# Optimization experiments

Hardware: AMD Instinct MI355X
Metric: run time of the kernel (lower is better)

Reference implementation:

```python
import jax, jax.numpy as jnp
import numpy as np

B, S, D, H = 4, 1024, 1024, 16
HD = D // H          # head space dim = 64
FF = 4 * D           # ffn hidden = 4096
EPS = 1e-6

# ---- Lorentz manifold helpers (curvature k=1: -t^2 + |s|^2 = -1) ----

def to_manifold(space):
    t = jnp.sqrt(jnp.sum(space * space, -1, keepdims=True) + 1.0)
    return jnp.concatenate([t, space], -1)

def l_inner(x, y):
    return -x[..., 0] * y[..., 0] + jnp.sum(x[..., 1:] * y[..., 1:], -1)

def project(z):
    # renormalize onto hyperboloid: z / sqrt(|<z,z>_L|)   (Lorentz midpoint / LResNet)
    d = jnp.sqrt(jnp.clip(-l_inner(z, z), EPS))
    return z / d[..., None]

def hyp_layernorm(x, g, b):
    s = x[..., 1:]
    mu = jnp.mean(s, -1, keepdims=True)
    var = jnp.var(s, -1, keepdims=True)
    s = (s - mu) * jax.lax.rsqrt(var + 1e-5) * g + b
    return to_manifold(s)

def apply_rope(xs, cos, sin):
    # xs [B,S,H,HD]; cos/sin [S,HD//2]; freqs broadcast as [1,S,1,HD//2]
    x2 = xs.reshape(*xs.shape[:-1], HD // 2, 2)
    c = cos[None, :, None, :]
    s = sin[None, :, None, :]
    xr = x2[..., 0] * c - x2[..., 1] * s
    xi = x2[..., 0] * s + x2[..., 1] * c
    return jnp.stack([xr, xi], -1).reshape(xs.shape)


def setup_inputs() -> dict:
    key = jax.random.key(0)
    ks = jax.random.split(key, 8)
    def w(k, shape, fan_in):
        return jax.random.normal(k, shape, jnp.float32) / np.sqrt(fan_in).astype(np.float32)
    x = to_manifold(0.5 * jax.random.normal(ks[0], (B, S, D), jnp.float32))
    pos = jnp.arange(S, dtype=jnp.float32)[:, None]
    inv = 1.0 / (10000.0 ** (jnp.arange(0, HD, 2, dtype=jnp.float32) / HD))
    ang = pos * inv[None, :]
    return {
        'x': x,
        'rope_cos': jnp.cos(ang), 'rope_sin': jnp.sin(ang),
        'norm1_g': jnp.ones((D,), jnp.float32), 'norm1_b': jnp.zeros((D,), jnp.float32),
        'Wq': w(ks[1], (H, D + 1, HD), D + 1), 'bq': jnp.zeros((H, HD), jnp.float32),
        'Wk': w(ks[2], (H, D + 1, HD), D + 1), 'bk': jnp.zeros((H, HD), jnp.float32),
        'Wv': w(ks[3], (H, D + 1, HD), D + 1), 'bv': jnp.zeros((H, HD), jnp.float32),
        'attn_scale': jnp.asarray(np.sqrt(HD), jnp.float32),
        'attn_bias': jnp.zeros((), jnp.float32),
        'Wo': w(ks[4], (H * (HD + 1), D), H * (HD + 1)), 'bo': jnp.zeros((D,), jnp.float32),
        'w_res1': jnp.asarray(1.0, jnp.float32),
        'norm2_g': jnp.ones((D,), jnp.float32), 'norm2_b': jnp.zeros((D,), jnp.float32),
        'W1': w(ks[5], (D + 1, FF), D + 1), 'b1': jnp.zeros((FF,), jnp.float32),
        'W2': w(ks[6], (FF + 1, D), FF + 1), 'b2': jnp.zeros((D,), jnp.float32),
        'w_res2': jnp.asarray(1.0, jnp.float32),
    }


def reference(x, rope_cos, rope_sin, norm1_g, norm1_b, Wq, bq, Wk, bk, Wv, bv,
              attn_scale, attn_bias, Wo, bo, w_res1, norm2_g, norm2_b,
              W1, b1, W2, b2, w_res2):
    # ---- pre-norm ----
    xn = hyp_layernorm(x, norm1_g, norm1_b)
    # ---- per-head Lorentz linear (space part), inline RoPE on q/k ----
    qs = jnp.einsum('bsd,hde->bshe', xn, Wq) + bq          # [B,S,H,HD]
    ksp = jnp.einsum('bsd,hde->bshe', xn, Wk) + bk
    vsp = jnp.einsum('bsd,hde->bshe', xn, Wv) + bv
    qs = apply_rope(qs, rope_cos, rope_sin)
    ksp = apply_rope(ksp, rope_cos, rope_sin)
    # hyperbolic normalization of q/k: unit space norm, time recomputed
    qs = qs * jax.lax.rsqrt(jnp.sum(qs * qs, -1, keepdims=True) + EPS)
    ksp = ksp * jax.lax.rsqrt(jnp.sum(ksp * ksp, -1, keepdims=True) + EPS)
    q = to_manifold(qs)                                    # [B,S,H,HD+1]
    k = to_manifold(ksp)
    v = to_manifold(vsp)
    # ---- curvature-aware scores: 2 + 2 <q,k>_L (neg sq Lorentz distance) ----
    sgn = jnp.concatenate([-jnp.ones((1,), q.dtype), jnp.ones((HD,), q.dtype)])
    cin = jnp.einsum('bshe,bthe->bhst', q * sgn, k)        # Minkowski inner [B,H,S,S]
    att = (2.0 + 2.0 * cin) / attn_scale + attn_bias
    P = jax.nn.softmax(att, axis=-1)
    # ---- Lorentz midpoint aggregation of values ----
    m = jnp.einsum('bhst,bthe->bshe', P, v)
    m = project(m)                                         # back onto hyperboloid
    # ---- heads concat + output Lorentz linear ----
    cat = m.reshape(B, S, H * (HD + 1))
    attn_out = to_manifold(cat @ Wo + bo)
    # ---- LResNet residual 1 ----
    x = project(x + w_res1 * attn_out)
    # ---- Lorentz FFN ----
    h = hyp_layernorm(x, norm2_g, norm2_b)
    h = to_manifold(jax.nn.gelu(h @ W1 + b1))
    mlp = to_manifold(h @ W2 + b2)
    # ---- LResNet residual 2 ----
    x = project(x + w_res2 * mlp)
    return x
```

## Files before the change

kernel.cpp:

```cpp
#include <hip/hip_runtime.h>
#include <hip/hip_bf16.h>

typedef __hip_bfloat16 bf16;
typedef __attribute__((ext_vector_type(8))) short short8;
typedef __attribute__((ext_vector_type(4))) float f32x4;

#define B_  4
#define S_  1024
#define H_  16
#define R_  4096
#define LD_ 1088

#define MBL 1048576L
#define OFF_WQKVT (0L)
#define OFF_WOT   (6684672L)
#define OFF_X2    (0L)
#define OFF_W1T   (9L*MBL)
#define OFF_W2T   (18L*MBL)
#define OFF_BIAS  (26L*MBL)
#define OFF_XNB   (27L*MBL + MBL/2)
#define OFF_MCAT  OFF_XNB
#define OFF_HBUF  OFF_XNB
#define OFF_QPS   (36L*MBL)
#define OFF_ARAW  OFF_QPS
#define OFF_KPS   (44L*MBL)
#define OFF_VT    (52L*MBL)
#define OFF_QT    (62L*MBL)
#define OFF_KT    (62L*MBL + 262144L)
#define OFF_HHBIG (44L*MBL)
#define OFF_MLPB  (76L*MBL)
#define OFF_HHC   (36L*MBL)
#define OFF_MLPF  (44L*MBL)
#define BQKV 0
#define BOF  16384
#define B1F  32768
#define B2F  65536
#define W2R0 81920
#define RCF  98304
#define RSNF 262144
#define SCLF 409600
#define TACC 425984
#define FLAG 458752

__device__ __forceinline__ bf16  f2bf(float v) { return __float2bfloat16(v); }
__device__ __forceinline__ float bf2f(bf16 v)  { return __bfloat162float(v); }
__device__ __forceinline__ unsigned short bf2s(float v) {
  return __builtin_bit_cast(unsigned short, __float2bfloat16(v));
}
__device__ __forceinline__ float ldu(const void* p, long i, int isbf) {
  return isbf ? bf2f(((const bf16*)p)[i]) : ((const float*)p)[i];
}
__device__ __forceinline__ void stu(void* p, long i, float v, int isbf) {
  if (isbf) ((bf16*)p)[i] = f2bf(v);
  else      ((float*)p)[i] = v;
}
__device__ __forceinline__ float gelu_f(float v) {
  const float u = 0.7978845608028654f * (v + 0.044715f * v * v * v);
  const float e = __expf(fminf(2.f * u, 80.f));
  return 0.5f * v * (1.f + (e - 1.f) / (e + 1.f));
}
__device__ __forceinline__ float bfu_lo(unsigned u) {
  return __builtin_bit_cast(float, u << 16);
}
__device__ __forceinline__ float bfu_hi(unsigned u) {
  return __builtin_bit_cast(float, u & 0xFFFF0000u);
}

__device__ __forceinline__ void gload16(const bf16* g, short* l) {
  __builtin_amdgcn_global_load_lds(
      (const __attribute__((address_space(1))) unsigned int*)g,
      (__attribute__((address_space(3))) unsigned int*)l, 16, 0, 0);
}

__global__ void detect_kernel(const unsigned* __restrict__ g, int* __restrict__ flag) {
  if (threadIdx.x == 0) flag[0] = (g[0] == 0x3F803F80u) ? 1 : 0;
}

__global__ __launch_bounds__(256) void zero16_kernel(uint4* __restrict__ p, int n16) {
  int i = blockIdx.x * 256 + threadIdx.x;
  if (i < n16) p[i] = uint4{0, 0, 0, 0};
}

__device__ __forceinline__ float bred_f(float v, float* sh) {
#pragma unroll
  for (int o = 32; o; o >>= 1) v += __shfl_xor(v, o);
  __syncthreads();
  if ((threadIdx.x & 63) == 0) sh[threadIdx.x >> 6] = v;
  __syncthreads();
  return sh[0] + sh[1] + sh[2] + sh[3];
}
__device__ __forceinline__ double bred_d(double v, double* sh) {
#pragma unroll
  for (int o = 32; o; o >>= 1) v += __shfl_xor(v, o);
  __syncthreads();
  if ((threadIdx.x & 63) == 0) sh[threadIdx.x >> 6] = v;
  __syncthreads();
  return sh[0] + sh[1] + sh[2] + sh[3];
}

__global__ __launch_bounds__(256) void mega_prep(
    const void* x, const void* rc, const void* rsn, const void* n1g, const void* n1b,
    const void* Wq, const void* bq, const void* Wk, const void* bk,
    const void* Wv, const void* bv, const void* scl, const void* ab,
    const void* Wo, const void* bo, const void* wr1,
    const void* W1, const void* b1, const void* W2, const void* b2, const void* wr2,
    char* bias_base, bf16* __restrict__ wqkvT, bf16* __restrict__ woT,
    bf16* __restrict__ w1T, bf16* __restrict__ w2T, bf16* __restrict__ xnb,
    const int* __restrict__ flag) {
  const int isbf = flag[0];
  __shared__ float tl[64][65];
  const int tid = threadIdx.x;
  int bid = blockIdx.x;
  if (bid < 297) {
    int i = bid * 256 + tid;
    float* bqkvf = (float*)(bias_base + BQKV);
    if (i < 1024)        { bqkvf[i] = ldu(bq, i, isbf); return; }
    if (i < 2048)        { bqkvf[i] = ldu(bk, i - 1024, isbf); return; }
    if (i < 3072)        { bqkvf[i] = ldu(bv, i - 2048, isbf); return; }
    if (i < 4096)        { ((float*)(bias_base + BOF))[i - 3072] = ldu(bo, i - 3072, isbf); return; }
    if (i < 8192)        { ((float*)(bias_base + B1F))[i - 4096] = ldu(b1, i - 4096, isbf); return; }
    if (i < 9216)        { ((float*)(bias_base + B2F))[i - 8192] = ldu(b2, i - 8192, isbf); return; }
    if (i < 10240)       { ((float*)(bias_base + W2R0))[i - 9216] = ldu(W2, i - 9216, isbf); return; }
    if (i < 10240+32768) { ((float*)(bias_base + RCF))[i - 10240] = ldu(rc, i - 10240, isbf); return; }
    if (i < 10240+65536) { ((float*)(bias_base + RSNF))[i - 43008] = ldu(rsn, i - 43008, isbf); return; }
    if (i == 75776)      { ((float*)(bias_base + SCLF))[0] = ldu(scl, 0, isbf); return; }
    if (i == 75777)      { ((float*)(bias_base + SCLF))[1] = ldu(ab, 0, isbf); return; }
    if (i == 75778)      { ((float*)(bias_base + SCLF))[2] = ldu(wr1, 0, isbf); return; }
    if (i == 75779)      { ((float*)(bias_base + SCLF))[3] = ldu(wr2, 0, isbf); return; }
    return;
  }
  bid -= 297;
  const int tx = tid & 63, tg = tid >> 6;
  if (bid < 816) {
    int k0 = (bid % 17) * 64, z = bid / 17;
    int mode = z >> 4, h = z & 15;
    const void* src = (mode == 0) ? Wq : (mode == 1) ? Wk : Wv;
    const long soff = (long)h * 1025 * 64;
    int base_n = mode * 1024 + h * 64;
    for (int i = tg; i < 64; i += 4) {
      int k = k0 + i;
      tl[i][tx] = (k < 1025) ? ldu(src, soff + (long)k * 64 + tx, isbf) : 0.f;
    }
    __syncthreads();
    for (int i = tg; i < 64; i += 4) {
      int k = k0 + tx;
      if (k < LD_) wqkvT[(long)(base_n + i) * LD_ + k] = f2bf(tl[tx][i]);
    }
    return;
  }
  bid -= 816;
  if (bid < 272) {
    int k0 = (bid % 17) * 64, n0 = (bid / 17) * 64;
    for (int i = tg; i < 64; i += 4) {
      int kp = k0 + i;
      float v = 0.f;
      if (kp < 1056) {
        int h = kp / 66, e = kp - h * 66;
        if (e < 65) v = ldu(Wo, (long)(h * 65 + e) * 1024 + n0 + tx, isbf);
      }
      tl[i][tx] = v;
    }
    __syncthreads();
    for (int i = tg; i < 64; i += 4) {
      int kp = k0 + tx;
      if (kp < LD_) woT[(long)(n0 + i) * LD_ + kp] = f2bf(tl[tx][i]);
    }
    return;
  }
  bid -= 272;
  if (bid < 1088) {
    int k0 = (bid % 17) * 64, n0 = (bid / 17) * 64;
    for (int i = tg; i < 64; i += 4) {
      int k = k0 + i;
      tl[i][tx] = (k < 1025) ? ldu(W1, (long)k * 4096 + n0 + tx, isbf) : 0.f;
    }
    __syncthreads();
    for (int i = tg; i < 64; i += 4) {
      int k = k0 + tx;
      if (k < LD_) w1T[(long)(n0 + i) * LD_ + k] = f2bf(tl[tx][i]);
    }
    return;
  }
  bid -= 1088;
  if (bid < 1024) {
    int k0 = (bid % 64) * 64, n0 = (bid / 64) * 64;
    for (int i = tg; i < 64; i += 4) {
      int k = k0 + i;
      tl[i][tx] = ldu(W2, 1024 + (long)k * 1024 + n0 + tx, isbf);
    }
    __syncthreads();
    for (int i = tg; i < 64; i += 4) {
      int k = k0 + tx;
      w2T[(long)(n0 + i) * 4096 + k] = f2bf(tl[tx][i]);
    }
    return;
  }
  bid -= 1024;
  {
    float* red = &tl[0][0];
    const long base = (long)bid * 1025;
    const long obase = (long)bid * LD_;
    float v[4];
#pragma unroll
    for (int i = 0; i < 4; i++) v[i] = ldu(x, base + 1 + tid * 4 + i, isbf);
    float s = 0.f, s2 = 0.f;
#pragma unroll
    for (int i = 0; i < 4; i++) { s += v[i]; s2 += v[i] * v[i]; }
    s  = bred_f(s,  red);
    s2 = bred_f(s2, red);
    const float mu  = s * (1.f / 1024.f);
    const float var = s2 * (1.f / 1024.f) - mu * mu;
    const float rs  = rsqrtf(var + 1e-5f);
    float n[4], ns = 0.f;
#pragma unroll
    for (int i = 0; i < 4; i++) {
      const int e = tid * 4 + i;
      n[i] = (v[i] - mu) * rs * ldu(n1g, e, isbf) + ldu(n1b, e, isbf);
      ns += n[i] * n[i];
    }
    ns = bred_f(ns, red);
    if (tid == 0) xnb[obase] = f2bf(sqrtf(ns + 1.f));
#pragma unroll
    for (int i = 0; i < 4; i++) xnb[obase + 1 + tid * 4 + i] = f2bf(n[i]);
    if (tid < 63) xnb[obase + 1025 + tid] = f2bf(0.f);
  }
}

__device__ __forceinline__ void gemm256_main(const bf16* __restrict__ A, int lda,
                                             const bf16* __restrict__ Bw, int ldb, int K,
                                             short (*__restrict__ As)[8192],
                                             short (*__restrict__ Bs)[8192],
                                             f32x4 (*acc)[4]) {
  const int tid = threadIdx.x, lane = tid & 63, wv = tid >> 6;
  const int quad = lane >> 4, q15 = lane & 15;
  const int wave_m = wv >> 2, wave_n = wv & 3;
  const int m0 = blockIdx.y * 256, n0 = blockIdx.x * 256;
  const int NT = K >> 5;
  const int u0 = tid, u1 = tid + 512;
  const int r0 = u0 >> 2, c0 = ((u0 & 3) ^ ((u0 >> 3) & 3)) * 8;
  const int r1 = u1 >> 2, c1 = ((u1 & 3) ^ ((u1 >> 3) & 3)) * 8;
  const bf16* pa0 = A + (long)(m0 + r0) * lda + c0;
  const bf16* pa1 = A + (long)(m0 + r1) * lda + c1;
  const bf16* pb0 = Bw + (long)(n0 + r0) * ldb + c0;
  const bf16* pb1 = Bw + (long)(n0 + r1) * ldb + c1;
  const int d0 = u0 * 8, d1 = u1 * 8;
  const int kswz = (quad ^ ((q15 >> 1) & 3)) * 8;
  const int arow = wave_m * 128 + q15;
  const int brow = wave_n * 64 + q15;
  gload16(pa0, As[0] + d0); gload16(pa1, As[0] + d1);
  gload16(pb0, Bs[0] + d0); gload16(pb1, Bs[0] + d1);
  pa0 += 32; pa1 += 32; pb0 += 32; pb1 += 32;
  gload16(pa0, As[1] + d0); gload16(pa1, As[1] + d1);
  gload16(pb0, Bs[1] + d0); gload16(pb1, Bs[1] + d1);
  pa0 += 32; pa1 += 32; pb0 += 32; pb1 += 32;
  asm volatile("s_waitcnt vmcnt(4)" ::: "memory");
  __builtin_amdgcn_s_barrier();
#pragma unroll 1
  for (int t = 0; t < NT; ++t) {
    const int buf = t & 3, sb = (t + 2) & 3;
    const short* ab = As[buf];
    const short* bb = Bs[buf];
    short8 af[4], bfr[4];
#pragma unroll
    for (int i = 0; i < 4; i++) {
      af[i]  = *(const short8*)(ab + (arow + i * 16) * 32 + kswz);
      bfr[i] = *(const short8*)(bb + (brow + i * 16) * 32 + kswz);
    }
    if (t + 2 < NT) {
      gload16(pa0, As[sb] + d0); gload16(pa1, As[sb] + d1);
      pa0 += 32; pa1 += 32;
    }
    __builtin_amdgcn_s_barrier();
    __builtin_amdgcn_s_setprio(1);
#pragma unroll
    for (int mi = 0; mi < 4; mi++)
#pragma unroll
      for (int ni = 0; ni < 4; ni++)
        acc[mi][ni] = __builtin_amdgcn_mfma_f32_16x16x32_bf16(af[mi], bfr[ni], acc[mi][ni], 0, 0, 0);
    __builtin_amdgcn_s_setprio(0);
    __builtin_amdgcn_s_barrier();
#pragma unroll
    for (int i = 0; i < 4; i++)
      af[i] = *(const short8*)(ab + (arow + 64 + i * 16) * 32 + kswz);
    if (t + 2 < NT) {
      gload16(pb0, Bs[sb] + d0); gload16(pb1, Bs[sb] + d1);
      pb0 += 32; pb1 += 32;
      asm volatile("s_waitcnt vmcnt(4)" ::: "memory");
    } else {
      asm volatile("s_waitcnt vmcnt(0)" ::: "memory");
    }
    __builtin_amdgcn_s_barrier();
    __builtin_amdgcn_s_setprio(1);
#pragma unroll
    for (int mi = 0; mi < 4; mi++)
#pragma unroll
      for (int ni = 0; ni < 4; ni++)
        acc[4 + mi][ni] = __builtin_amdgcn_mfma_f32_16x16x32_bf16(af[mi], bfr[ni], acc[4 + mi][ni], 0, 0, 0);
    __builtin_amdgcn_s_setprio(0);
    __builtin_amdgcn_s_barrier();
  }
}

template <int EPI>
__global__ __launch_bounds__(512) void gemm256(const bf16* __restrict__ A, int lda,
                                               const bf16* __restrict__ Bw, int ldb, int K,
                                               const float* __restrict__ bias,
                                               void* __restrict__ Cv, int ldc, int accf) {
  __shared__ __align__(16) short As[4][8192];
  __shared__ __align__(16) short Bs[4][8192];
  f32x4 acc[8][4] = {};
  gemm256_main(A, lda, Bw, ldb, K, As, Bs, acc);
  const int tid = threadIdx.x, lane = tid & 63, wv = tid >> 6;
  const int quad = lane >> 4, q15 = lane & 15;
  const int wave_m = wv >> 2, wave_n = wv & 3;
  const int m0 = blockIdx.y * 256, n0 = blockIdx.x * 256;
#pragma unroll
  for (int j = 0; j < 8; j++) {
#pragma unroll
    for (int r = 0; r < 4; r++) {
      const int m = m0 + wave_m * 128 + (j >> 2) * 64 + (j & 3) * 16 + quad * 4 + r;
#pragma unroll
      for (int ni = 0; ni < 4; ni++) {
        const int n = n0 + wave_n * 64 + ni * 16 + q15;
        float v = acc[j][ni][r] + (bias ? bias[n] : 0.f);
        const long idx = (long)m * ldc + n;
        if (EPI == 0) {
          float* Cf = (float*)Cv;
          if (accf) v += Cf[idx];
          Cf[idx] = v;
        } else if (EPI == 1) {
          ((bf16*)Cv)[idx] = f2bf(v);
        } else {
          ((bf16*)Cv)[idx] = f2bf(gelu_f(v));
        }
      }
    }
  }
}

__global__ __launch_bounds__(512) void gemm_qkv256(const bf16* __restrict__ A,
                                                   const bf16* __restrict__ Wt,
                                                   const char* __restrict__ bias_base,
                                                   bf16* __restrict__ qPs, float* __restrict__ qtc,
                                                   bf16* __restrict__ kPs, float* __restrict__ ktc,
                                                   bf16* __restrict__ vT) {
  __shared__ __align__(16) short As[4][8192];
  __shared__ __align__(16) short Bs[4][8192];
  f32x4 acc[8][4] = {};
  gemm256_main(A, LD_, Wt, LD_, LD_, As, Bs, acc);
  const int tid = threadIdx.x, lane = tid & 63, wv = tid >> 6;
  const int quad = lane >> 4, q15 = lane & 15;
  const int wave_m = wv >> 2, wave_n = wv & 3;
  const int m0 = blockIdx.y * 256, n0 = blockIdx.x * 256;
  const float* bqkvf = (const float*)(bias_base + BQKV);
  const float* rcf   = (const float*)(bias_base + RCF);
  const float* rsnf  = (const float*)(bias_base + RSNF);
  const int hg = (n0 >> 6) + wave_n;
  const int mode = hg >> 4, h = hg & 15;
  const int nb = hg * 64;
#pragma unroll
  for (int j = 0; j < 8; j++) {
#pragma unroll
    for (int r = 0; r < 4; r++) {
      const int m = m0 + wave_m * 128 + (j >> 2) * 64 + (j & 3) * 16 + quad * 4 + r;
      const int bb = m >> 10, s = m & 1023;
      const int bh = bb * H_ + h;
      float v[4];
#pragma unroll
      for (int ns = 0; ns < 4; ns++) v[ns] = acc[j][ns][r] + bqkvf[nb + ns * 16 + q15];
      if (mode < 2) {
#pragma unroll
        for (int ns = 0; ns < 4; ns++) {
          const int eg = ns * 16 + q15;
          const int jj = eg >> 1;
          const float c = rcf[s * 32 + jj], sn = rsnf[s * 32 + jj];
          const float p = __shfl_xor(v[ns], 1);
          v[ns] = ((eg & 1) == 0) ? (v[ns] * c - p * sn) : (p * sn + v[ns] * c);
        }
      }
      float ss = v[0] * v[0] + v[1] * v[1] + v[2] * v[2] + v[3] * v[3];
#pragma unroll
      for (int o = 8; o; o >>= 1) ss += __shfl_xor(ss, o);
      if (mode == 0) {
        const float sc = rsqrtf(ss + 1e-6f);
        const long rb2 = (long)(bh * 1024 + s) * 64;
#pragma unroll
        for (int ns = 0; ns < 4; ns++) qPs[rb2 + ns * 16 + q15] = f2bf(v[ns] * sc);
        if (q15 == 0) qtc[bh * 1024 + s] = sqrtf(ss / (ss + 1e-6f) + 1.f);
      } else if (mode == 1) {
        const float sc = rsqrtf(ss + 1e-6f);
        const long rb2 = (long)(bh * 1024 + s) * 64;
#pragma unroll
        for (int ns = 0; ns < 4; ns++) kPs[rb2 + ns * 16 + q15] = f2bf(v[ns] * sc);
        if (q15 == 0) ktc[bh * 1024 + s] = sqrtf(ss / (ss + 1e-6f) + 1.f);
      } else {
        const long vb = (long)bh * 81920;
#pragma unroll
        for (int ns = 0; ns < 4; ns++) vT[vb + (long)(1 + ns * 16 + q15) * 1024 + s] = f2bf(v[ns]);
        if (q15 == 0) vT[vb + s] = f2bf(sqrtf(ss + 1.f));
      }
    }
  }
}

template <int EPI, bool SS>
__global__ __launch_bounds__(256) void mfma_gemm(const bf16* __restrict__ A, int lda,
                                                 const bf16* __restrict__ Bw, int ldb, int K,
                                                 const float* __restrict__ bias,
                                                 void* __restrict__ Cv, int ldc, int accf,
                                                 float* __restrict__ tacc) {
  __shared__ __align__(16) short As[2][128 * 32];
  __shared__ __align__(16) short Bs[2][64 * 32];
  const int tid = threadIdx.x, lane = tid & 63, wv = tid >> 6;
  const int quad = lane >> 4, q15 = lane & 15;
  const int wave_m = wv & 1, wave_n = wv >> 1;
  const int n0 = blockIdx.x * 64, m0 = blockIdx.y * 128;
  const int sa0 = wv * 128 + lane, sa1 = sa0 + 64;
  const int ra0 = sa0 >> 2, ca0 = (sa0 & 3) ^ (ra0 & 3);
  const int ra1 = sa1 >> 2, ca1 = (sa1 & 3) ^ (ra1 & 3);
  const int rb = tid >> 2, cb = (tid & 3) ^ (rb & 3);
  const int kswz = (quad ^ (q15 & 3)) * 8;
  const bf16* pa0 = A + (long)(m0 + ra0) * lda + ca0 * 8;
  const bf16* pa1 = A + (long)(m0 + ra1) * lda + ca1 * 8;
  const bf16* pb  = Bw + (long)(n0 + rb) * ldb + cb * 8;
  f32x4 acc[4][2] = {};
  for (int k0 = 0; k0 < K; k0 += 64) {
#pragma unroll
    for (int p = 0; p < 2; p++) {
      gload16(pa0 + p * 32, As[p] + sa0 * 8);
      gload16(pa1 + p * 32, As[p] + sa1 * 8);
      gload16(pb + p * 32, Bs[p] + tid * 8);
    }
    pa0 += 64; pa1 += 64; pb += 64;
    __syncthreads();
#pragma unroll
    for (int p = 0; p < 2; p++) {
      short8 af[4], bfr[2];
#pragma unroll
      for (int i = 0; i < 4; i++)
        af[i] = *(const short8*)(As[p] + (wave_m * 64 + i * 16 + q15) * 32 + kswz);
#pragma unroll
      for (int i = 0; i < 2; i++)
        bfr[i] = *(const short8*)(Bs[p] + (wave_n * 32 + i * 16 + q15) * 32 + kswz);
#pragma unroll
      for (int mi = 0; mi < 4; mi++)
#pragma unroll
        for (int ni = 0; ni < 2; ni++)
          acc[mi][ni] = __builtin_amdgcn_mfma_f32_16x16x32_bf16(af[mi], bfr[ni], acc[mi][ni], 0, 0, 0);
    }
    __syncthreads();
  }
#pragma unroll
  for (int mi = 0; mi < 4; mi++) {
#pragma unroll
    for (int r = 0; r < 4; r++) {
      const int m = m0 + wave_m * 64 + mi * 16 + quad * 4 + r;
      float s2 = 0.f;
#pragma unroll
      for (int ni = 0; ni < 2; ni++) {
        const int n = n0 + wave_n * 32 + ni * 16 + q15;
        float v = acc[mi][ni][r] + (bias ? bias[n] : 0.f);
        const long idx = (long)m * ldc + n;
        if (EPI == 0) {
          float* Cf = (float*)Cv;
          if (accf) v += Cf[idx];
          Cf[idx] = v;
        } else if (EPI == 1) {
          ((bf16*)Cv)[idx] = f2bf(v);
        } else {
          v = gelu_f(v);
          ((bf16*)Cv)[idx] = f2bf(v);
        }
        if (SS) s2 += v * v;
      }
      if (SS) {
        s2 += __shfl_xor(s2, 1);
        s2 += __shfl_xor(s2, 2);
        s2 += __shfl_xor(s2, 4);
        s2 += __shfl_xor(s2, 8);
        if (q15 == 0) atomicAdd(tacc + m, s2);
      }
    }
  }
}

__global__ __launch_bounds__(256) void attn_kernel(const bf16* __restrict__ qPs,
                                                   const float* __restrict__ qtc,
                                                   const bf16* __restrict__ kPs,
                                                   const float* __restrict__ ktc,
                                                   const bf16* __restrict__ vT,
                                                   const float* __restrict__ scalf,
                                                   bf16* __restrict__ mcat) {
  __shared__ __align__(16) short kbuf[64 * 72];
  __shared__ __align__(16) short vbuf[80 * 72];
  __shared__ __align__(16) short pbuf[64 * 72];
  __shared__ float tkl[64];
  const int tid = threadIdx.x, lane = tid & 63, wv = tid >> 6;
  const int quad = lane >> 4, q15 = lane & 15;
  const int id = blockIdx.x;
  const int cxd = id & 7, jj_ = id >> 3;
  const int bh = cxd * 8 + (jj_ & 7), qt_ = jj_ >> 3;
  const float inv_scale = 1.f / scalf[0];
  const long qrow = (long)(bh * 1024 + qt_ * 64 + wv * 16 + q15) * 64;
  const short8 aq0 = *(const short8*)(qPs + qrow + quad * 8);
  const short8 aq1 = *(const short8*)(qPs + qrow + 32 + quad * 8);
  float tqr[4];
#pragma unroll
  for (int r = 0; r < 4; r++) tqr[r] = qtc[bh * 1024 + qt_ * 64 + wv * 16 + quad * 4 + r];
  f32x4 out[5];
#pragma unroll
  for (int mt = 0; mt < 5; mt++) out[mt] = f32x4{0, 0, 0, 0};
  float lip[4] = {0.f, 0.f, 0.f, 0.f};
  const int srcl = (q15 >> 2) << 4;
  for (int kt = 0; kt < 16; kt++) {
    __syncthreads();
#pragma unroll
    for (int c = 0; c < 2; c++) {
      const int id2 = c * 256 + tid, row = id2 >> 3, off = id2 & 7;
      *(uint4*)(kbuf + row * 72 + off * 8) =
          *(const uint4*)(kPs + (long)(bh * 1024 + kt * 64 + row) * 64 + off * 8);
    }
#pragma unroll
    for (int c = 0; c < 3; c++) {
      const int id2 = c * 256 + tid;
      if (id2 < 640) {
        const int row = id2 >> 3, off = id2 & 7;
        *(uint4*)(vbuf + row * 72 + off * 8) =
            *(const uint4*)(vT + (long)bh * 81920 + (long)row * 1024 + kt * 64 + off * 8);
      }
    }
    if (tid < 64) tkl[tid] = ktc[bh * 1024 + kt * 64 + tid];
    __syncthreads();
    f32x4 sacc[4] = {f32x4{0,0,0,0}, f32x4{0,0,0,0}, f32x4{0,0,0,0}, f32x4{0,0,0,0}};
#pragma unroll
    for (int ns = 0; ns < 4; ns++) {
      short8 b0 = *(const short8*)(kbuf + (ns * 16 + q15) * 72 + quad * 8);
      short8 b1 = *(const short8*)(kbuf + (ns * 16 + q15) * 72 + 32 + quad * 8);
      sacc[ns] = __builtin_amdgcn_mfma_f32_16x16x32_bf16(aq0, b0, sacc[ns], 0, 0, 0);
      sacc[ns] = __builtin_amdgcn_mfma_f32_16x16x32_bf16(aq1, b1, sacc[ns], 0, 0, 0);
    }
#pragma unroll
    for (int ns = 0; ns < 4; ns++) {
      const float tk = tkl[ns * 16 + q15];
#pragma unroll
      for (int r = 0; r < 4; r++) {
        const float pv = __expf((2.f + 2.f * (sacc[ns][r] - tqr[r] * tk)) * inv_scale);
        lip[r] += pv;
        pbuf[(wv * 16 + quad * 4 + r) * 72 + ns * 16 + q15] = (short)bf2s(pv);
      }
    }
#pragma unroll
    for (int mt = 0; mt < 5; mt++)
#pragma unroll
      for (int kc = 0; kc < 2; kc++) {
        short8 av = *(const short8*)(vbuf + (mt * 16 + q15) * 72 + kc * 32 + quad * 8);
        short8 bp = *(const short8*)(pbuf + (wv * 16 + q15) * 72 + kc * 32 + quad * 8);
        out[mt] = __builtin_amdgcn_mfma_f32_16x16x32_bf16(av, bp, out[mt], 0, 0, 0);
      }
  }
  {
#pragma unroll
    for (int o = 8; o; o >>= 1)
#pragma unroll
      for (int r = 0; r < 4; r++) lip[r] += __shfl_xor(lip[r], o);
    float linv[4];
#pragma unroll
    for (int r = 0; r < 4; r++) linv[r] = 1.f / lip[r];
    const float t0 = __shfl(linv[0], srcl), t1 = __shfl(linv[1], srcl);
    const float t2 = __shfl(linv[2], srcl), t3 = __shfl(linv[3], srcl);
    const int rr = q15 & 3;
    const float lv = (rr == 0) ? t0 : (rr == 1) ? t1 : (rr == 2) ? t2 : t3;
#pragma unroll
    for (int mt = 0; mt < 5; mt++)
#pragma unroll
      for (int j = 0; j < 4; j++) out[mt][j] *= lv;
  }
  float part = 0.f;
#pragma unroll
  for (int mt = 0; mt < 5; mt++)
#pragma unroll
    for (int j = 0; j < 4; j++) {
      const int e = mt * 16 + quad * 4 + j;
      const float vv = out[mt][j] * out[mt][j];
      part += (e == 0) ? vv : -vv;
    }
  part += __shfl_xor(part, 16);
  part += __shfl_xor(part, 32);
  const float dinv = rsqrtf(fmaxf(part, 1e-6f));
  __syncthreads();
  short* obuf = vbuf;
  const int qrow_l = wv * 16 + q15;
#pragma unroll
  for (int mt = 0; mt < 5; mt++)
#pragma unroll
    for (int j = 0; j < 4; j++) {
      const int e = mt * 16 + quad * 4 + j;
      if (e <= 64) obuf[qrow_l * 72 + e] = (short)bf2s(out[mt][j] * dinv);
    }
  if (quad == 1) obuf[qrow_l * 72 + 65] = 0;
  __syncthreads();
  const int b = bh >> 4, h = bh & 15;
  const long outbase = ((long)b * 1024 + qt_ * 64) * LD_ + h * 66;
  for (int i = tid; i < 64 * 33; i += 256) {
    const int row = i / 33, p = i - row * 33;
    *(unsigned*)(mcat + outbase + (long)row * LD_ + p * 2) =
        *(const unsigned*)(obuf + row * 72 + p * 2);
  }
  if (h == 15) {
    const long zb = ((long)b * 1024 + qt_ * 64) * LD_ + 1056;
    for (int i = tid; i < 64 * 16; i += 256) {
      const int row = i >> 4, p = i & 15;
      *(unsigned*)(mcat + zb + (long)row * LD_ + p * 2) = 0u;
    }
  }
}

__global__ __launch_bounds__(256) void final_fix_kernel(const float* __restrict__ t_acc,
                                                        const float* __restrict__ w2r0,
                                                        const float* __restrict__ b2f,
                                                        float* __restrict__ mlp) {
  const int m = blockIdx.x;
  const float t = sqrtf(1.f + t_acc[m]);
  float* row = mlp + (long)m * 1024;
  for (int n = threadIdx.x; n < 1024; n += 256) row[n] += t * w2r0[n] + b2f[n];
}

__global__ __launch_bounds__(256) void final_fix_big(const bf16* __restrict__ hh,
                                                     const float* __restrict__ w2r0,
                                                     const float* __restrict__ b2f,
                                                     float* __restrict__ mlp) {
  __shared__ float red[4];
  const int m = blockIdx.x;
  const uint4* r4 = (const uint4*)(hh + (long)m * 4096);
  float ss = 0.f;
  for (int i = threadIdx.x; i < 512; i += 256) {
    const uint4 u = r4[i];
    const unsigned a[4] = {u.x, u.y, u.z, u.w};
#pragma unroll
    for (int j = 0; j < 4; j++) {
      const float lo = bfu_lo(a[j]), hi = bfu_hi(a[j]);
      ss += lo * lo + hi * hi;
    }
  }
  ss = bred_f(ss, red);
  const float t = sqrtf(1.f + ss);
  float* row = mlp + (long)m * 1024;
  for (int n = threadIdx.x; n < 1024; n += 256) row[n] += t * w2r0[n] + b2f[n];
}

__global__ __launch_bounds__(256) void proj_ln_kernel(
    const void* __restrict__ x, const bf16* __restrict__ c,
    const float* __restrict__ scalf, int widx,
    const void* __restrict__ g, const void* __restrict__ b,
    bf16* __restrict__ x2, bf16* __restrict__ hbuf, const int* __restrict__ flag) {
  const int isbf = flag[0];
  __shared__ double redd[4];
  __shared__ float redf[4];
  const long bx = (long)blockIdx.x * 1025;
  const long bc = (long)blockIdx.x * 1024;
  const long ob = (long)blockIdx.x * LD_;
  const int tid = threadIdx.x;
  const double w = (double)scalf[widx];
  const float x0 = ldu(x, bx, isbf);
  float xs[4], cv[4];
#pragma unroll
  for (int i = 0; i < 4; i++) {
    xs[i] = ldu(x, bx + 1 + tid * 4 + i, isbf);
    cv[i] = bf2f(c[bc + tid * 4 + i]);
  }
  double cc = 0.0, xx = 0.0, xc = 0.0, sx = 0.0, sc_ = 0.0;
#pragma unroll
  for (int i = 0; i < 4; i++) {
    cc += (double)cv[i] * cv[i];
    xx += (double)xs[i] * xs[i];
    xc += (double)xs[i] * cv[i];
    sx += (double)xs[i];
    sc_ += (double)cv[i];
  }
  cc = bred_d(cc, redd);
  xx = bred_d(xx, redd);
  xc = bred_d(xc, redd);
  sx = bred_d(sx, redd);
  sc_ = bred_d(sc_, redd);
  const double t   = sqrt(1.0 + cc);
  const double lxx = (double)x0 * x0 - xx;
  const double xm  = -(double)x0 * t + xc;
  double d2 = lxx + w * w - 2.0 * w * xm;
  if (d2 < 1e-6) d2 = 1e-6;
  const double dinv = 1.0 / sqrt(d2);
  if (tid == 0) x2[bx] = f2bf((float)(((double)x0 + w * t) * dinv));
  float z[4];
#pragma unroll
  for (int i = 0; i < 4; i++) {
    z[i] = (float)(((double)xs[i] + w * cv[i]) * dinv);
    x2[bx + 1 + tid * 4 + i] = f2bf(z[i]);
  }
  const float sumz  = (float)((sx + w * sc_) * dinv);
  const float sumsq = (float)((xx + 2.0 * w * xc + w * w * cc) * dinv * dinv);
  const float mu  = sumz * (1.f / 1024.f);
  const float var = sumsq * (1.f / 1024.f) - mu * mu;
  const float rs  = rsqrtf(var + 1e-5f);
  float n[4], ns = 0.f;
#pragma unroll
  for (int i = 0; i < 4; i++) {
    const int e = tid * 4 + i;
    n[i] = (z[i] - mu) * rs * ldu(g, e, isbf) + ldu(b, e, isbf);
    ns += n[i] * n[i];
  }
  ns = bred_f(ns, redf);
  if (tid == 0) hbuf[ob] = f2bf(sqrtf(ns + 1.f));
#pragma unroll
  for (int i = 0; i < 4; i++) hbuf[ob + 1 + tid * 4 + i] = f2bf(n[i]);
  if (tid < 63) hbuf[ob + 1025 + tid] = f2bf(0.f);
}

__global__ __launch_bounds__(256) void res_project_kernel(
    const void* __restrict__ x, int xtag, const void* __restrict__ c, int ctag,
    const float* __restrict__ scalf, int widx, void* __restrict__ out, int otag,
    const int* __restrict__ flag) {
  const int isbf = flag[0];
  const int xb = (xtag == 2) ? isbf : xtag;
  const int cb2 = (ctag == 2) ? isbf : ctag;
  const int ob = (otag == 2) ? isbf : otag;
  __shared__ double red[4];
  const long bx = (long)blockIdx.x * 1025;
  const long bc = (long)blockIdx.x * 1024;
  const int tid = threadIdx.x;
  const double w = (double)scalf[widx];
  const float x0 = ldu(x, bx, xb);
  float xs[4], cv[4];
#pragma unroll
  for (int i = 0; i < 4; i++) {
    xs[i] = ldu(x, bx + 1 + tid * 4 + i, xb);
    cv[i] = ldu(c, bc + tid * 4 + i, cb2);
  }
  double cc = 0.0, xx = 0.0, xc = 0.0;
#pragma unroll
  for (int i = 0; i < 4; i++) {
    cc += (double)cv[i] * cv[i];
    xx += (double)xs[i] * xs[i];
    xc += (double)xs[i] * cv[i];
  }
  cc = bred_d(cc, red);
  xx = bred_d(xx, red);
  xc = bred_d(xc, red);
  const double t   = sqrt(1.0 + cc);
  const double lxx = (double)x0 * x0 - xx;
  const double xm  = -(double)x0 * t + xc;
  double d2 = lxx + w * w - 2.0 * w * xm;
  if (d2 < 1e-6) d2 = 1e-6;
  const double dinv = 1.0 / sqrt(d2);
  if (tid == 0) stu(out, bx, (float)(((double)x0 + w * t) * dinv), ob);
#pragma unroll
  for (int i = 0; i < 4; i++)
    stu(out, bx + 1 + tid * 4 + i, (float)(((double)xs[i] + w * cv[i]) * dinv), ob);
}

extern "C" void kernel_launch(void* const* d_in, const int* in_sizes, int n_in,
                              void* d_out, int out_size, void* d_ws, size_t ws_size,
                              hipStream_t stream) {
  char* w = (char*)d_ws;
  char* bias_base = w + OFF_BIAS;
  int* flag = (int*)(bias_base + FLAG);
  float* tacc = (float*)(bias_base + TACC);
  const float* scalf = (const float*)(bias_base + SCLF);
  const bool big = ws_size >= (size_t)92 * MBL;
  char* mlp_off = big ? (w + OFF_MLPB) : (w + OFF_MLPF);

  detect_kernel<<<1, 64, 0, stream>>>((const unsigned*)d_in[3], flag);
  zero16_kernel<<<4, 256, 0, stream>>>((uint4*)tacc, 1024);

  mega_prep<<<7593, 256, 0, stream>>>(
      d_in[0], d_in[1], d_in[2], d_in[3], d_in[4], d_in[5], d_in[6], d_in[7], d_in[8],
      d_in[9], d_in[10], d_in[11], d_in[12], d_in[13], d_in[14], d_in[15], d_in[18],
      d_in[19], d_in[20], d_in[21], d_in[22], bias_base, (bf16*)(w + OFF_WQKVT),
      (bf16*)(w + OFF_WOT), (bf16*)(w + OFF_W1T), (bf16*)(w + OFF_W2T),
      (bf16*)(w + OFF_XNB), flag);

  gemm_qkv256<<<dim3(12, 16), 512, 0, stream>>>(
      (const bf16*)(w + OFF_XNB), (const bf16*)(w + OFF_WQKVT), bias_base,
      (bf16*)(w + OFF_QPS), (float*)(w + OFF_QT), (bf16*)(w + OFF_KPS),
      (float*)(w + OFF_KT), (bf16*)(w + OFF_VT));
  attn_kernel<<<1024, 256, 0, stream>>>(
      (const bf16*)(w + OFF_QPS), (const float*)(w + OFF_QT), (const bf16*)(w + OFF_KPS),
      (const float*)(w + OFF_KT), (const bf16*)(w + OFF_VT), scalf, (bf16*)(w + OFF_MCAT));
  mfma_gemm<1, false><<<dim3(16, 32), 256, 0, stream>>>(
      (const bf16*)(w + OFF_MCAT), LD_, (const bf16*)(w + OFF_WOT), LD_, LD_,
      (const float*)(bias_base + BOF), w + OFF_ARAW, 1024, 0, nullptr);
  proj_ln_kernel<<<R_, 256, 0, stream>>>(d_in[0], (const bf16*)(w + OFF_ARAW), scalf, 2,
                                         d_in[16], d_in[17], (bf16*)(w + OFF_X2),
                                         (bf16*)(w + OFF_HBUF), flag);
  if (big) {
    gemm256<2><<<dim3(16, 16), 512, 0, stream>>>(
        (const bf16*)(w + OFF_HBUF), LD_, (const bf16*)(w + OFF_W1T), LD_, LD_,
        (const float*)(bias_base + B1F), w + OFF_HHBIG, 4096, 0);
    mfma_gemm<0, false><<<dim3(16, 32), 256, 0, stream>>>(
        (const bf16*)(w + OFF_HHBIG), 4096, (const bf16*)(w + OFF_W2T), 4096, 4096,
        nullptr, mlp_off, 1024, 0, nullptr);
    final_fix_big<<<R_, 256, 0, stream>>>((const bf16*)(w + OFF_HHBIG),
                                          (const float*)(bias_base + W2R0),
                                          (const float*)(bias_base + B2F),
                                          (float*)mlp_off);
  } else {
    for (int c = 0; c < 4; c++) {
      mfma_gemm<2, true><<<dim3(16, 32), 256, 0, stream>>>(
          (const bf16*)(w + OFF_HBUF), LD_, (const bf16*)(w + OFF_W1T) + (long)c * 1024 * LD_,
          LD_, LD_, (const float*)(bias_base + B1F) + c * 1024, w + OFF_HHC, 1024, 0, tacc);
      mfma_gemm<0, false><<<dim3(16, 32), 256, 0, stream>>>(
          (const bf16*)(w + OFF_HHC), 1024, (const bf16*)(w + OFF_W2T) + c * 1024, 4096, 1024,
          nullptr, mlp_off, 1024, c > 0 ? 1 : 0, nullptr);
    }
    final_fix_kernel<<<R_, 256, 0, stream>>>(tacc, (const float*)(bias_base + W2R0),
                                             (const float*)(bias_base + B2F),
                                             (float*)mlp_off);
  }
  res_project_kernel<<<R_, 256, 0, stream>>>(w + OFF_X2, 1, mlp_off, 0, scalf, 3,
                                             d_out, 2, flag);
}
```

Before: 479.1 us.

## Restructure 256x256 GEMM mainloop to K=64 double-buffered tiles with four-phase MFMA schedule

Result: faster. 465.7 us (-2.8%).

```diff
diff --git a/kernel.cpp b/kernel.cpp
--- a/kernel.cpp
+++ b/kernel.cpp
@@ -72,6 +72,12 @@
       (__attribute__((address_space(3))) unsigned int*)l, 16, 0, 0);
 }
 
+#define MFMA_(acc_, a_, b_) acc_ = __builtin_amdgcn_mfma_f32_16x16x32_bf16(a_, b_, acc_, 0, 0, 0)
+#define LGKM_GUARD() do { \
+    asm volatile("s_waitcnt lgkmcnt(0)" ::: "memory"); \
+    __builtin_amdgcn_sched_barrier(0); \
+  } while (0)
+
 __global__ void detect_kernel(const unsigned* __restrict__ g, int* __restrict__ flag) {
   if (threadIdx.x == 0) flag[0] = (g[0] == 0x3F803F80u) ? 1 : 0;
 }
@@ -226,77 +232,131 @@
   }
 }
 
-__device__ __forceinline__ void gemm256_main(const bf16* __restrict__ A, int lda,
-                                             const bf16* __restrict__ Bw, int ldb, int K,
-                                             short (*__restrict__ As)[8192],
-                                             short (*__restrict__ Bs)[8192],
-                                             f32x4 (*acc)[4]) {
+#define BUFS 16384
+__device__ __forceinline__ void g256_main(const bf16* __restrict__ A, int lda,
+                                          const bf16* __restrict__ Bw, int ldb, int K,
+                                          short* __restrict__ AsB, short* __restrict__ BsB,
+                                          f32x4 (*acc)[4]) {
   const int tid = threadIdx.x, lane = tid & 63, wv = tid >> 6;
   const int quad = lane >> 4, q15 = lane & 15;
-  const int wave_m = wv >> 2, wave_n = wv & 3;
+  const int wm = wv >> 2, wn = wv & 3;
   const int m0 = blockIdx.y * 256, n0 = blockIdx.x * 256;
-  const int NT = K >> 5;
-  const int u0 = tid, u1 = tid + 512;
-  const int r0 = u0 >> 2, c0 = ((u0 & 3) ^ ((u0 >> 3) & 3)) * 8;
-  const int r1 = u1 >> 2, c1 = ((u1 & 3) ^ ((u1 >> 3) & 3)) * 8;
-  const bf16* pa0 = A + (long)(m0 + r0) * lda + c0;
-  const bf16* pa1 = A + (long)(m0 + r1) * lda + c1;
-  const bf16* pb0 = Bw + (long)(n0 + r0) * ldb + c0;
-  const bf16* pb1 = Bw + (long)(n0 + r1) * ldb + c1;
-  const int d0 = u0 * 8, d1 = u1 * 8;
-  const int kswz = (quad ^ ((q15 >> 1) & 3)) * 8;
-  const int arow = wave_m * 128 + q15;
-  const int brow = wave_n * 64 + q15;
-  gload16(pa0, As[0] + d0); gload16(pa1, As[0] + d1);
-  gload16(pb0, Bs[0] + d0); gload16(pb1, Bs[0] + d1);
-  pa0 += 32; pa1 += 32; pb0 += 32; pb1 += 32;
-  gload16(pa0, As[1] + d0); gload16(pa1, As[1] + d1);
-  gload16(pb0, Bs[1] + d0); gload16(pb1, Bs[1] + d1);
-  pa0 += 32; pa1 += 32; pb0 += 32; pb1 += 32;
+  const int NT = K >> 6;
+  const int srow = tid >> 3;
+  const int sunit = (tid & 7) ^ (srow & 7);
+  const bf16* pa[4]; const bf16* pb[4];
+#pragma unroll
+  for (int j = 0; j < 4; j++) {
+    pa[j] = A  + (long)(m0 + j * 64 + srow) * lda + sunit * 8;
+    pb[j] = Bw + (long)(n0 + j * 64 + srow) * ldb + sunit * 8;
+  }
+#pragma unroll
+  for (int j = 0; j < 4; j++) gload16(pa[j], AsB + (j * 512 + tid) * 8);
+#pragma unroll
+  for (int j = 0; j < 4; j++) gload16(pb[j], BsB + (j * 512 + tid) * 8);
+#pragma unroll
+  for (int j = 0; j < 4; j++) { pb[j] += 64; gload16(pb[j], BsB + BUFS + (j * 512 + tid) * 8); }
+#pragma unroll
+  for (int j = 0; j < 4; j++) { pa[j] += 64; pb[j] += 64; }
   asm volatile("s_waitcnt vmcnt(4)" ::: "memory");
   __builtin_amdgcn_s_barrier();
+  const int aoff = wm * 128 * 64 + q15 * 64;
+  const int boff = wn * 64 * 64 + q15 * 64;
+  const int rd0 = ((quad) ^ (q15 & 7)) * 8;
+  const int rd1 = ((4 + quad) ^ (q15 & 7)) * 8;
 #pragma unroll 1
-  for (int t = 0; t < NT; ++t) {
-    const int buf = t & 3, sb = (t + 2) & 3;
-    const short* ab = As[buf];
-    const short* bb = Bs[buf];
-    short8 af[4], bfr[4];
-#pragma unroll
-    for (int i = 0; i < 4; i++) {
-      af[i]  = *(const short8*)(ab + (arow + i * 16) * 32 + kswz);
-      bfr[i] = *(const short8*)(bb + (brow + i * 16) * 32 + kswz);
-    }
-    if (t + 2 < NT) {
-      gload16(pa0, As[sb] + d0); gload16(pa1, As[sb] + d1);
-      pa0 += 32; pa1 += 32;
+  for (int t = 0; t < NT; t++) {
+    const int c = t & 1;
+    const short* Ab = AsB + c * BUFS;
+    const short* Bb = BsB + c * BUFS;
+    short* Ast = AsB + (c ^ 1) * BUFS;
+    short* Bst = BsB + c * BUFS;
+    short8 af[4][2], b01[2][2], b23[2][2];
+#pragma unroll
+    for (int f = 0; f < 4; f++) {
+      af[f][0] = *(const short8*)(Ab + aoff + f * 16 * 64 + rd0);
+      af[f][1] = *(const short8*)(Ab + aoff + f * 16 * 64 + rd1);
+    }
+#pragma unroll
+    for (int g = 0; g < 2; g++) {
+      b01[g][0] = *(const short8*)(Bb + boff + g * 16 * 64 + rd0);
+      b01[g][1] = *(const short8*)(Bb + boff + g * 16 * 64 + rd1);
+    }
+    if (t + 1 < NT) {
+#pragma unroll
+      for (int j = 0; j < 4; j++) gload16(pa[j], Ast + (j * 512 + tid) * 8);
+#pragma unroll
+      for (int j = 0; j < 4; j++) pa[j] += 64;
     }
     __builtin_amdgcn_s_barrier();
     __builtin_amdgcn_s_setprio(1);
 #pragma unroll
-    for (int mi = 0; mi < 4; mi++)
-#pragma unroll
-      for (int ni = 0; ni < 4; ni++)
-        acc[mi][ni] = __builtin_amdgcn_mfma_f32_16x16x32_bf16(af[mi], bfr[ni], acc[mi][ni], 0, 0, 0);
+    for (int kk = 0; kk < 2; kk++)
+#pragma unroll
+      for (int f = 0; f < 4; f++)
+#pragma unroll
+        for (int g = 0; g < 2; g++)
+          MFMA_(acc[f][g], af[f][kk], b01[g][kk]);
     __builtin_amdgcn_s_setprio(0);
     __builtin_amdgcn_s_barrier();
 #pragma unroll
-    for (int i = 0; i < 4; i++)
-      af[i] = *(const short8*)(ab + (arow + 64 + i * 16) * 32 + kswz);
-    if (t + 2 < NT) {
-      gload16(pb0, Bs[sb] + d0); gload16(pb1, Bs[sb] + d1);
-      pb0 += 32; pb1 += 32;
-      asm volatile("s_waitcnt vmcnt(4)" ::: "memory");
-    } else {
-      asm volatile("s_waitcnt vmcnt(0)" ::: "memory");
+    for (int g = 0; g < 2; g++) {
+      b23[g][0] = *(const short8*)(Bb + boff + (32 + g * 16) * 64 + rd0);
+      b23[g][1] = *(const short8*)(Bb + boff + (32 + g * 16) * 64 + rd1);
     }
     __builtin_amdgcn_s_barrier();
     __builtin_amdgcn_s_setprio(1);
 #pragma unroll
-    for (int mi = 0; mi < 4; mi++)
-#pragma unroll
-      for (int ni = 0; ni < 4; ni++)
-        acc[4 + mi][ni] = __builtin_amdgcn_mfma_f32_16x16x32_bf16(af[mi], bfr[ni], acc[4 + mi][ni], 0, 0, 0);
+    for (int kk = 0; kk < 2; kk++)
+#pragma unroll
+      for (int f = 0; f < 4; f++)
+#pragma unroll
+        for (int g = 0; g < 2; g++)
+          MFMA_(acc[f][2 + g], af[f][kk], b23[g][kk]);
     __builtin_amdgcn_s_setprio(0);
+    LGKM_GUARD();
+    __builtin_amdgcn_s_barrier();
+#pragma unroll
+    for (int f = 0; f < 4; f++) {
+      af[f][0] = *(const short8*)(Ab + aoff + (64 + f * 16) * 64 + rd0);
+      af[f][1] = *(const short8*)(Ab + aoff + (64 + f * 16) * 64 + rd1);
+    }
+    if (t + 2 < NT) {
+      gload16(pb[0], Bst + (0 * 512 + tid) * 8);
+      gload16(pb[1], Bst + (1 * 512 + tid) * 8);
+    }
+    __builtin_amdgcn_s_barrier();
+    __builtin_amdgcn_s_setprio(1);
+#pragma unroll
+    for (int kk = 0; kk < 2; kk++)
+#pragma unroll
+      for (int f = 0; f < 4; f++)
+#pragma unroll
+        for (int g = 0; g < 2; g++)
+          MFMA_(acc[4 + f][g], af[f][kk], b01[g][kk]);
+    __builtin_amdgcn_s_setprio(0);
+    __builtin_amdgcn_s_barrier();
+    if (t + 2 < NT) {
+      gload16(pb[2], Bst + (2 * 512 + tid) * 8);
+      gload16(pb[3], Bst + (3 * 512 + tid) * 8);
+#pragma unroll
+      for (int j = 0; j < 4; j++) pb[j] += 64;
+    }
+    __builtin_amdgcn_s_setprio(1);
+#pragma unroll
+    for (int kk = 0; kk < 2; kk++)
+#pragma unroll
+      for (int f = 0; f < 4; f++)
+#pragma unroll
+        for (int g = 0; g < 2; g++)
+          MFMA_(acc[4 + f][2 + g], af[f][kk], b23[g][kk]);
+    __builtin_amdgcn_s_setprio(0);
+    if (t + 2 < NT) {
+      asm volatile("s_waitcnt vmcnt(4) lgkmcnt(0)" ::: "memory");
+    } else {
+      asm volatile("s_waitcnt vmcnt(0) lgkmcnt(0)" ::: "memory");
+    }
+    __builtin_amdgcn_sched_barrier(0);
     __builtin_amdgcn_s_barrier();
   }
 }
@@ -306,10 +366,10 @@
                                                const bf16* __restrict__ Bw, int ldb, int K,
                                                const float* __restrict__ bias,
                                                void* __restrict__ Cv, int ldc, int accf) {
-  __shared__ __align__(16) short As[4][8192];
-  __shared__ __align__(16) short Bs[4][8192];
+  __shared__ __align__(16) short As[2][BUFS];
+  __shared__ __align__(16) short Bs[2][BUFS];
   f32x4 acc[8][4] = {};
-  gemm256_main(A, lda, Bw, ldb, K, As, Bs, acc);
+  g256_main(A, lda, Bw, ldb, K, &As[0][0], &Bs[0][0], acc);
   const int tid = threadIdx.x, lane = tid & 63, wv = tid >> 6;
   const int quad = lane >> 4, q15 = lane & 15;
   const int wave_m = wv >> 2, wave_n = wv & 3;
@@ -318,7 +378,7 @@
   for (int j = 0; j < 8; j++) {
 #pragma unroll
     for (int r = 0; r < 4; r++) {
-      const int m = m0 + wave_m * 128 + (j >> 2) * 64 + (j & 3) * 16 + quad * 4 + r;
+      const int m = m0 + wave_m * 128 + j * 16 + quad * 4 + r;
 #pragma unroll
       for (int ni = 0; ni < 4; ni++) {
         const int n = n0 + wave_n * 64 + ni * 16 + q15;
@@ -344,10 +404,10 @@
                                                    bf16* __restrict__ qPs, float* __restrict__ qtc,
                                                    bf16* __restrict__ kPs, float* __restrict__ ktc,
                                                    bf16* __restrict__ vT) {
-  __shared__ __align__(16) short As[4][8192];
-  __shared__ __align__(16) short Bs[4][8192];
+  __shared__ __align__(16) short As[2][BUFS];
+  __shared__ __align__(16) short Bs[2][BUFS];
   f32x4 acc[8][4] = {};
-  gemm256_main(A, LD_, Wt, LD_, LD_, As, Bs, acc);
+  g256_main(A, LD_, Wt, LD_, LD_, &As[0][0], &Bs[0][0], acc);
   const int tid = threadIdx.x, lane = tid & 63, wv = tid >> 6;
   const int quad = lane >> 4, q15 = lane & 15;
   const int wave_m = wv >> 2, wave_n = wv & 3;
@@ -362,7 +422,7 @@
   for (int j = 0; j < 8; j++) {
 #pragma unroll
     for (int r = 0; r < 4; r++) {
-      const int m = m0 + wave_m * 128 + (j >> 2) * 64 + (j & 3) * 16 + quad * 4 + r;
+      const int m = m0 + wave_m * 128 + j * 16 + quad * 4 + r;
       const int bb = m >> 10, s = m & 1023;
       const int bh = bb * H_ + h;
       float v[4];
```
